# Performance work log

Measured on AMD Instinct MI355X. Metric: run time of the kernel, lower is better.

## Reference

```python
import jax, jax.numpy as jnp
import numpy as np

EPS = 1e-8  # torch F.cosine_similarity default eps


def setup_inputs() -> dict:
    key = jax.random.key(0)
    k1, k2 = jax.random.split(key)
    B, D, C = 8192, 1024, 1000
    x = jax.random.normal(k1, (B, D), dtype=jnp.float32)
    W = jax.random.normal(k2, (D, C), dtype=jnp.float32) * 0.02
    b = jnp.zeros((C,), dtype=jnp.float32)
    return {"x": x, "W": W, "b": b}


def reference(x, W, b):
    B = x.shape[0]
    # classifier logits -> softmax probs
    logits = x @ W + b                              # [B, C]
    logp = jax.nn.log_softmax(logits, axis=1)       # [B, C]
    pred = jnp.exp(logp)
    # per-row sum of p * log p (negative entropy), matches pred*log(pred) loop
    loss = jnp.sum(pred * logp, axis=-1)            # [B]
    # per-row mean cosine similarity against all rows (incl. self)
    norms = jnp.maximum(jnp.linalg.norm(x, axis=1, keepdims=True), EPS)
    xn = x / norms                                  # [B, D]
    sim = xn @ xn.T                                 # [B, B]
    weight = jnp.sum(sim, axis=1) / B               # [B]
    return loss * weight
```

## Files before the change

### kernel.cpp

```cpp
#include <hip/hip_runtime.h>
#include <hip/hip_bf16.h>
#include <cstdint>
#include <cstddef>

typedef __attribute__((ext_vector_type(8))) short bf16x8;
typedef __attribute__((ext_vector_type(4))) float f32x4;

__device__ __forceinline__ unsigned short f2bf(float f) {
  union { float f; unsigned u; } v; v.f = f;
  unsigned r = v.u + 0x7FFFu + ((v.u >> 16) & 1u);
  return (unsigned short)(r >> 16);
}

__device__ __forceinline__ float bf2f(unsigned short h) {
  union { float f; unsigned u; } c; c.u = ((unsigned)h) << 16;
  return c.f;
}

__device__ __forceinline__ void gload_lds16(const void* g, void* l) {
  __builtin_amdgcn_global_load_lds(
      (const __attribute__((address_space(1))) unsigned int*)g,
      (__attribute__((address_space(3))) unsigned int*)l, 16, 0, 0);
}

__global__ __launch_bounds__(1024) void k01_prep(const float* __restrict__ W,
                                                 unsigned short* __restrict__ Wt,
                                                 const float* __restrict__ x,
                                                 unsigned short* __restrict__ xbf,
                                                 float* __restrict__ rnorm,
                                                 float* __restrict__ sp) {
  __shared__ __align__(16) char sm[82176];
  int tid = threadIdx.x;
  int b = blockIdx.x;
  int lane = tid & 63;
  int wid = tid >> 6;

  int k0 = (b & 15) * 64;
  int c0 = (b >> 4) * 64;
  int tx = tid & 63;
  int ty = tid >> 6;
  float wreg[4];
#pragma unroll
  for (int i = 0; i < 4; ++i) {
    int c = c0 + tx;
    wreg[i] = (c < 1000) ? W[(size_t)(k0 + i * 16 + ty) * 1000 + c] : 0.f;
  }

  {
    float (*sblk)[1024] = (float(*)[1024])sm;
    int row0 = b * 32 + wid * 2;
    const float4* xr0 = (const float4*)(x + (size_t)row0 * 1024);
    const float4* xr1 = (const float4*)(x + (size_t)(row0 + 1) * 1024);
    float4 v[2][4];
#pragma unroll
    for (int j = 0; j < 4; ++j) v[0][j] = xr0[lane + j * 64];
#pragma unroll
    for (int j = 0; j < 4; ++j) v[1][j] = xr1[lane + j * 64];
    float ss0 = 0.f, ss1 = 0.f;
#pragma unroll
    for (int j = 0; j < 4; ++j) {
      ss0 += v[0][j].x * v[0][j].x + v[0][j].y * v[0][j].y +
             v[0][j].z * v[0][j].z + v[0][j].w * v[0][j].w;
      ss1 += v[1][j].x * v[1][j].x + v[1][j].y * v[1][j].y +
             v[1][j].z * v[1][j].z + v[1][j].w * v[1][j].w;
    }
#pragma unroll
    for (int m = 1; m < 64; m <<= 1) {
      ss0 += __shfl_xor(ss0, m);
      ss1 += __shfl_xor(ss1, m);
    }
    float rn0 = 1.f / fmaxf(sqrtf(ss0), 1e-8f);
    float rn1 = 1.f / fmaxf(sqrtf(ss1), 1e-8f);
    if (lane == 0) {
      rnorm[row0] = rn0;
      rnorm[row0 + 1] = rn1;
    }
    float4 sacc[4];
#pragma unroll
    for (int j = 0; j < 4; ++j) {
      ushort4 h0, h1;
      h0.x = f2bf(v[0][j].x); h0.y = f2bf(v[0][j].y);
      h0.z = f2bf(v[0][j].z); h0.w = f2bf(v[0][j].w);
      h1.x = f2bf(v[1][j].x); h1.y = f2bf(v[1][j].y);
      h1.z = f2bf(v[1][j].z); h1.w = f2bf(v[1][j].w);
      ((ushort4*)(xbf + (size_t)row0 * 1024))[lane + j * 64] = h0;
      ((ushort4*)(xbf + (size_t)(row0 + 1) * 1024))[lane + j * 64] = h1;
      sacc[j].x = v[0][j].x * rn0 + v[1][j].x * rn1;
      sacc[j].y = v[0][j].y * rn0 + v[1][j].y * rn1;
      sacc[j].z = v[0][j].z * rn0 + v[1][j].z * rn1;
      sacc[j].w = v[0][j].w * rn0 + v[1][j].w * rn1;
    }
#pragma unroll
    for (int j = 0; j < 4; ++j) ((float4*)sblk[wid])[j * 64 + lane] = sacc[j];
    __syncthreads();
    float acc = 0.f;
#pragma unroll
    for (int w = 0; w < 16; ++w) acc += sblk[w][tid];
    sp[(size_t)b * 1024 + tid] = acc;
  }

  {
    float (*tile)[65] = (float(*)[65])(sm + 65536);
#pragma unroll
    for (int i = 0; i < 4; ++i) tile[i * 16 + ty][tx] = wreg[i];
    __syncthreads();
#pragma unroll
    for (int i = 0; i < 4; ++i) {
      int ct = i * 16 + ty;
      Wt[(size_t)(c0 + ct) * 1024 + (k0 + tx)] = f2bf(tile[tx][ct]);
    }
  }
}

__global__ __launch_bounds__(256) void k2_sred(const float* __restrict__ sp,
                                               float* __restrict__ s) {
  __shared__ float red[4][64];
  int t = threadIdx.x;
  int dd = t & 63;
  int g = t >> 6;
  int d = blockIdx.x * 64 + dd;
  float acc = 0.f;
#pragma unroll 8
  for (int b = g * 64; b < g * 64 + 64; ++b) acc += sp[(size_t)b * 1024 + d];
  red[g][dd] = acc;
  __syncthreads();
  if (g == 0) s[d] = red[0][dd] + red[1][dd] + red[2][dd] + red[3][dd];
}

__global__ __launch_bounds__(256) void k3_gemm(const unsigned short* __restrict__ xbf,
                                               const unsigned short* __restrict__ wt,
                                               const float* __restrict__ bias,
                                               float* __restrict__ pm,
                                               float* __restrict__ pz,
                                               float* __restrict__ ps) {
  __shared__ __align__(16) char lds[65536];

  int tid = threadIdx.x;
  int lane = tid & 63;
  int wid = tid >> 6;
  int wc = wid & 1;
  int wr = wid >> 1;
  int cb = blockIdx.x >> 6;
  int rb = blockIdx.x & 63;
  int C0 = cb * 128;
  int R0 = rb * 128;

  float bv[4][4];
#pragma unroll
  for (int mf = 0; mf < 4; ++mf)
#pragma unroll
    for (int q = 0; q < 4; ++q) {
      int cls_g = C0 + wc * 64 + mf * 16 + (lane >> 4) * 4 + q;
      bv[mf][q] = (cls_g < 1000) ? bias[cls_g] : -1e30f;
    }
  f32x4 acc[4][4];
#pragma unroll
  for (int mf = 0; mf < 4; ++mf)
#pragma unroll
    for (int nf = 0; nf < 4; ++nf)
#pragma unroll
      for (int q = 0; q < 4; ++q) acc[mf][nf][q] = bv[mf][q];

  const char* gA = (const char*)(wt + (size_t)C0 * 1024);
  const char* gB = (const char*)(xbf + (size_t)R0 * 1024);
  int grow = (tid >> 3) & 7;
  int gswz = ((tid & 7) ^ grow) << 4;

  auto stage = [&](int kt, int bb) {
    char* lA = lds + bb * 32768;
    char* lB = lA + 16384;
#pragma unroll
    for (int i = 0; i < 4; ++i) {
      size_t row = i * 32 + (tid >> 3);
      gload_lds16(gA + row * 2048 + kt * 128 + gswz, lA + i * 4096 + tid * 16);
    }
#pragma unroll
    for (int i = 0; i < 4; ++i) {
      size_t row = i * 32 + (tid >> 3);
      gload_lds16(gB + row * 2048 + kt * 128 + gswz, lB + i * 4096 + tid * 16);
    }
  };

  int rsw = (lane & 7) << 4;
  int kcol = (lane >> 4) * 16;

  stage(0, 0);
  __syncthreads();
  int cur = 0;
  for (int t = 0; t < 16; ++t) {
    if (t < 15) stage(t + 1, cur ^ 1);
    const char* A = lds + cur * 32768;
    const char* B = A + 16384;
    bf16x8 a[4][2], bb[4][2];
#pragma unroll
    for (int mf = 0; mf < 4; ++mf)
#pragma unroll
      for (int ks = 0; ks < 2; ++ks)
        a[mf][ks] = *(const bf16x8*)(A + (wc * 64 + mf * 16 + (lane & 15)) * 128 +
                                     ((ks * 64 + kcol) ^ rsw));
#pragma unroll
    for (int nf = 0; nf < 4; ++nf)
#pragma unroll
      for (int ks = 0; ks < 2; ++ks)
        bb[nf][ks] = *(const bf16x8*)(B + (wr * 64 + nf * 16 + (lane & 15)) * 128 +
                                      ((ks * 64 + kcol) ^ rsw));
    __builtin_amdgcn_s_setprio(1);
#pragma unroll
    for (int ks = 0; ks < 2; ++ks)
#pragma unroll
      for (int mf = 0; mf < 4; ++mf)
#pragma unroll
        for (int nf = 0; nf < 4; ++nf)
          acc[mf][nf] = __builtin_amdgcn_mfma_f32_16x16x32_bf16(a[mf][ks], bb[nf][ks],
                                                                acc[mf][nf], 0, 0, 0);
    __builtin_amdgcn_s_setprio(0);
    __syncthreads();
    cur ^= 1;
  }

  float* mm = (float*)lds;
  float* zz = mm + 256;
  float* sv = zz + 256;
#pragma unroll
  for (int nf = 0; nf < 4; ++nf) {
    float m1 = -1e30f;
#pragma unroll
    for (int mf = 0; mf < 4; ++mf)
#pragma unroll
      for (int q = 0; q < 4; ++q) m1 = fmaxf(m1, acc[mf][nf][q]);
    m1 = fmaxf(m1, __shfl_xor(m1, 16));
    m1 = fmaxf(m1, __shfl_xor(m1, 32));
    float z1 = 0.f, s1 = 0.f;
#pragma unroll
    for (int mf = 0; mf < 4; ++mf)
#pragma unroll
      for (int q = 0; q < 4; ++q) {
        float tt = acc[mf][nf][q] - m1;
        float e = expf(tt);
        z1 += e;
        s1 += e * tt;
      }
    z1 += __shfl_xor(z1, 16); z1 += __shfl_xor(z1, 32);
    s1 += __shfl_xor(s1, 16); s1 += __shfl_xor(s1, 32);
    if (lane < 16) {
      int r = wr * 64 + nf * 16 + lane;
      mm[wc * 128 + r] = m1;
      zz[wc * 128 + r] = z1;
      sv[wc * 128 + r] = s1;
    }
  }
  __syncthreads();
  if (tid < 128) {
    float m0 = mm[tid], mA = mm[128 + tid];
    float z0 = zz[tid], zA = zz[128 + tid];
    float s0 = sv[tid], sA = sv[128 + tid];
    float M = fmaxf(m0, mA);
    float e0 = expf(m0 - M), e1 = expf(mA - M);
    float Z = z0 * e0 + zA * e1;
    float S = e0 * (s0 + (m0 - M) * z0) + e1 * (sA + (mA - M) * zA);
    size_t o = (size_t)cb * 8192 + R0 + tid;
    pm[o] = M;
    pz[o] = Z;
    ps[o] = S;
  }
}

__global__ __launch_bounds__(256) void k4_final(const unsigned short* __restrict__ xbf,
                                                const float* __restrict__ s,
                                                const float* __restrict__ rnorm,
                                                const float* __restrict__ pm,
                                                const float* __restrict__ pz,
                                                const float* __restrict__ ps,
                                                float* __restrict__ out) {
  int tid = threadIdx.x;
  int wid = tid >> 6, lane = tid & 63;
  int row = blockIdx.x * 4 + wid;
  const bf16x8* xr = (const bf16x8*)(xbf + (size_t)row * 1024);
  const float4* s4 = (const float4*)s;
  float dot = 0.f;
#pragma unroll
  for (int j = 0; j < 2; ++j) {
    bf16x8 v = xr[lane + j * 64];
    float4 sa = s4[(lane + j * 64) * 2];
    float4 sb = s4[(lane + j * 64) * 2 + 1];
    dot += bf2f((unsigned short)v[0]) * sa.x + bf2f((unsigned short)v[1]) * sa.y +
           bf2f((unsigned short)v[2]) * sa.z + bf2f((unsigned short)v[3]) * sa.w +
           bf2f((unsigned short)v[4]) * sb.x + bf2f((unsigned short)v[5]) * sb.y +
           bf2f((unsigned short)v[6]) * sb.z + bf2f((unsigned short)v[7]) * sb.w;
  }
#pragma unroll
  for (int m = 1; m < 64; m <<= 1) dot += __shfl_xor(dot, m);
  if (lane == 0) {
    float mv[8], zv[8], svv[8];
    float M = -1e30f;
#pragma unroll
    for (int c = 0; c < 8; ++c) {
      mv[c] = pm[(size_t)c * 8192 + row];
      zv[c] = pz[(size_t)c * 8192 + row];
      svv[c] = ps[(size_t)c * 8192 + row];
      M = fmaxf(M, mv[c]);
    }
    float Z = 0.f, S = 0.f;
#pragma unroll
    for (int c = 0; c < 8; ++c) {
      float e = expf(mv[c] - M);
      Z += zv[c] * e;
      S += e * (svv[c] + (mv[c] - M) * zv[c]);
    }
    float loss = S / Z - logf(Z);
    out[row] = loss * dot * rnorm[row] * (1.f / 8192.f);
  }
}

extern "C" void kernel_launch(void* const* d_in, const int* in_sizes, int n_in,
                              void* d_out, int out_size, void* d_ws, size_t ws_size,
                              hipStream_t stream) {
  (void)in_sizes; (void)n_in; (void)out_size; (void)ws_size;
  const float* x = (const float*)d_in[0];
  const float* W = (const float*)d_in[1];
  const float* b = (const float*)d_in[2];
  float* out = (float*)d_out;
  char* ws = (char*)d_ws;

  unsigned short* Wt = (unsigned short*)(ws + 0);
  unsigned short* xbf = (unsigned short*)(ws + 2097152);
  float* rnorm = (float*)(ws + 18874368);
  float* s = (float*)(ws + 18907136);
  float* sp = (float*)(ws + 18915328);
  float* pm = (float*)(ws + 18915328);
  float* pz = (float*)(ws + 18915328 + 262144);
  float* ps = (float*)(ws + 18915328 + 524288);

  k01_prep<<<256, 1024, 0, stream>>>(W, Wt, x, xbf, rnorm, sp);
  k2_sred<<<16, 256, 0, stream>>>(sp, s);
  k3_gemm<<<512, 256, 0, stream>>>(xbf, Wt, b, pm, pz, ps);
  k4_final<<<2048, 256, 0, stream>>>(xbf, s, rnorm, pm, pz, ps, out);
}
```

Measured before the change: 52.58 us.

## Pre-pack W into MFMA fragment layout and load A operand directly from global

The prep kernel now writes the transposed bf16 weights in a per-fragment layout, so each lane's 16-byte MFMA A operand is contiguous in global memory. The GEMM kernel drops LDS staging for the weight operand and loads A fragments straight from global/L2, which halves LDS use and removes the A global-to-LDS copies and LDS reads. The risk is that the direct global loads are not double-buffered, so their latency may be exposed in the main loop, and every wave in a block now fetches its own A fragments instead of sharing one staged copy.

```diff
diff --git a/kernel.cpp b/kernel.cpp
--- a/kernel.cpp
+++ b/kernel.cpp
@@ -24,12 +24,12 @@
 }
 
 __global__ __launch_bounds__(1024) void k01_prep(const float* __restrict__ W,
-                                                 unsigned short* __restrict__ Wt,
+                                                 unsigned short* __restrict__ wtf,
                                                  const float* __restrict__ x,
                                                  unsigned short* __restrict__ xbf,
                                                  float* __restrict__ rnorm,
                                                  float* __restrict__ sp) {
-  __shared__ __align__(16) char sm[82176];
+  __shared__ __align__(16) char sm[83968];
   int tid = threadIdx.x;
   int b = blockIdx.x;
   int lane = tid & 63;
@@ -100,14 +100,26 @@
   }
 
   {
-    float (*tile)[65] = (float(*)[65])(sm + 65536);
-#pragma unroll
-    for (int i = 0; i < 4; ++i) tile[i * 16 + ty][tx] = wreg[i];
+    float (*tile2)[72] = (float(*)[72])(sm + 65536);
+#pragma unroll
+    for (int i = 0; i < 4; ++i) tile2[tx][i * 16 + ty] = wreg[i];
     __syncthreads();
-#pragma unroll
-    for (int i = 0; i < 4; ++i) {
-      int ct = i * 16 + ty;
-      Wt[(size_t)(c0 + ct) * 1024 + (k0 + tx)] = f2bf(tile[tx][ct]);
+    if (tid < 512) {
+      int fi = tid >> 6;
+      int l = tid & 63;
+      int cf = fi >> 1;
+      int kf = fi & 1;
+      int r2 = cf * 16 + (l & 15);
+      int c2 = kf * 32 + (l >> 4) * 8;
+      float4 va = *(const float4*)&tile2[r2][c2];
+      float4 vb = *(const float4*)&tile2[r2][c2 + 4];
+      uint4 o;
+      o.x = (unsigned)f2bf(va.x) | ((unsigned)f2bf(va.y) << 16);
+      o.y = (unsigned)f2bf(va.z) | ((unsigned)f2bf(va.w) << 16);
+      o.z = (unsigned)f2bf(vb.x) | ((unsigned)f2bf(vb.y) << 16);
+      o.w = (unsigned)f2bf(vb.z) | ((unsigned)f2bf(vb.w) << 16);
+      size_t fg = (size_t)(c0 / 16 + cf) * 32 + (k0 / 32 + kf);
+      *(uint4*)((char*)wtf + fg * 1024 + (size_t)l * 16) = o;
     }
   }
 }
@@ -128,12 +140,12 @@
 }
 
 __global__ __launch_bounds__(256) void k3_gemm(const unsigned short* __restrict__ xbf,
-                                               const unsigned short* __restrict__ wt,
+                                               const unsigned short* __restrict__ wtf,
                                                const float* __restrict__ bias,
                                                float* __restrict__ pm,
                                                float* __restrict__ pz,
                                                float* __restrict__ ps) {
-  __shared__ __align__(16) char lds[65536];
+  __shared__ __align__(16) char lds[32768];
 
   int tid = threadIdx.x;
   int lane = tid & 63;
@@ -161,19 +173,12 @@
 #pragma unroll
       for (int q = 0; q < 4; ++q) acc[mf][nf][q] = bv[mf][q];
 
-  const char* gA = (const char*)(wt + (size_t)C0 * 1024);
   const char* gB = (const char*)(xbf + (size_t)R0 * 1024);
   int grow = (tid >> 3) & 7;
   int gswz = ((tid & 7) ^ grow) << 4;
 
-  auto stage = [&](int kt, int bb) {
-    char* lA = lds + bb * 32768;
-    char* lB = lA + 16384;
-#pragma unroll
-    for (int i = 0; i < 4; ++i) {
-      size_t row = i * 32 + (tid >> 3);
-      gload_lds16(gA + row * 2048 + kt * 128 + gswz, lA + i * 4096 + tid * 16);
-    }
+  auto stageB = [&](int kt, int bb) {
+    char* lB = lds + bb * 16384;
 #pragma unroll
     for (int i = 0; i < 4; ++i) {
       size_t row = i * 32 + (tid >> 3);
@@ -181,23 +186,24 @@
     }
   };
 
+  const char* gAf = (const char*)wtf +
+                    ((size_t)(cb * 8 + wc * 4) * 32) * 1024 + (size_t)lane * 16;
+
   int rsw = (lane & 7) << 4;
   int kcol = (lane >> 4) * 16;
 
-  stage(0, 0);
+  stageB(0, 0);
   __syncthreads();
   int cur = 0;
   for (int t = 0; t < 16; ++t) {
-    if (t < 15) stage(t + 1, cur ^ 1);
-    const char* A = lds + cur * 32768;
-    const char* B = A + 16384;
+    if (t < 15) stageB(t + 1, cur ^ 1);
     bf16x8 a[4][2], bb[4][2];
 #pragma unroll
     for (int mf = 0; mf < 4; ++mf)
 #pragma unroll
       for (int ks = 0; ks < 2; ++ks)
-        a[mf][ks] = *(const bf16x8*)(A + (wc * 64 + mf * 16 + (lane & 15)) * 128 +
-                                     ((ks * 64 + kcol) ^ rsw));
+        a[mf][ks] = *(const bf16x8*)(gAf + (size_t)(mf * 32 + t * 2 + ks) * 1024);
+    const char* B = lds + cur * 16384;
 #pragma unroll
     for (int nf = 0; nf < 4; ++nf)
 #pragma unroll
@@ -322,7 +328,7 @@
   float* out = (float*)d_out;
   char* ws = (char*)d_ws;
 
-  unsigned short* Wt = (unsigned short*)(ws + 0);
+  unsigned short* wtf = (unsigned short*)(ws + 0);
   unsigned short* xbf = (unsigned short*)(ws + 2097152);
   float* rnorm = (float*)(ws + 18874368);
   float* s = (float*)(ws + 18907136);
@@ -331,8 +337,8 @@
   float* pz = (float*)(ws + 18915328 + 262144);
   float* ps = (float*)(ws + 18915328 + 524288);
 
-  k01_prep<<<256, 1024, 0, stream>>>(W, Wt, x, xbf, rnorm, sp);
+  k01_prep<<<256, 1024, 0, stream>>>(W, wtf, x, xbf, rnorm, sp);
   k2_sred<<<16, 256, 0, stream>>>(sp, s);
-  k3_gemm<<<512, 256, 0, stream>>>(xbf, Wt, b, pm, pz, ps);
+  k3_gemm<<<512, 256, 0, stream>>>(xbf, wtf, b, pm, pz, ps);
   k4_final<<<2048, 256, 0, stream>>>(xbf, s, rnorm, pm, pz, ps, out);
 }
```

New measurement: 54.14 us. +3.0%, slower.

## Fold column-sum dot product into logits GEMM as extra class row

Applied to the files above, without the earlier changes.

The column sum vector s is written as bf16 into padding row 1000 of the transposed weight matrix, so the logits GEMM also computes x·s for every row in an otherwise unused class slot. That value is extracted before the softmax reductions and masked out. The final kernel then only combines the partial softmax stats with the precomputed dot, so it no longer re-reads the bf16 x matrix. This relies on Wt padding rows existing and on the bias-slot initialisation handling class 1000, and it adds one extra barrier in the GEMM epilogue.

```diff
diff --git a/kernel.cpp b/kernel.cpp
--- a/kernel.cpp
+++ b/kernel.cpp
@@ -113,7 +113,8 @@
 }
 
 __global__ __launch_bounds__(256) void k2_sred(const float* __restrict__ sp,
-                                               float* __restrict__ s) {
+                                               float* __restrict__ s,
+                                               unsigned short* __restrict__ Wt) {
   __shared__ float red[4][64];
   int t = threadIdx.x;
   int dd = t & 63;
@@ -124,7 +125,11 @@
   for (int b = g * 64; b < g * 64 + 64; ++b) acc += sp[(size_t)b * 1024 + d];
   red[g][dd] = acc;
   __syncthreads();
-  if (g == 0) s[d] = red[0][dd] + red[1][dd] + red[2][dd] + red[3][dd];
+  if (g == 0) {
+    float sv = red[0][dd] + red[1][dd] + red[2][dd] + red[3][dd];
+    s[d] = sv;
+    Wt[(size_t)1000 * 1024 + d] = f2bf(sv);
+  }
 }
 
 __global__ __launch_bounds__(256) void k3_gemm(const unsigned short* __restrict__ xbf,
@@ -132,7 +137,8 @@
                                                const float* __restrict__ bias,
                                                float* __restrict__ pm,
                                                float* __restrict__ pz,
-                                               float* __restrict__ ps) {
+                                               float* __restrict__ ps,
+                                               float* __restrict__ pd) {
   __shared__ __align__(16) char lds[65536];
 
   int tid = threadIdx.x;
@@ -151,7 +157,7 @@
 #pragma unroll
     for (int q = 0; q < 4; ++q) {
       int cls_g = C0 + wc * 64 + mf * 16 + (lane >> 4) * 4 + q;
-      bv[mf][q] = (cls_g < 1000) ? bias[cls_g] : -1e30f;
+      bv[mf][q] = (cls_g < 1000) ? bias[cls_g] : ((cls_g == 1000) ? 0.f : -1e30f);
     }
   f32x4 acc[4][4];
 #pragma unroll
@@ -218,9 +224,19 @@
     cur ^= 1;
   }
 
+  if (cb == 7 && wc == 1 && ((lane >> 4) == 2)) {
+#pragma unroll
+    for (int nf = 0; nf < 4; ++nf) {
+      int r = wr * 64 + nf * 16 + (lane & 15);
+      pd[(size_t)rb * 128 + r] = acc[2][nf][0];
+      acc[2][nf][0] = -1e30f;
+    }
+  }
+
   float* mm = (float*)lds;
   float* zz = mm + 256;
   float* sv = zz + 256;
+  __syncthreads();
 #pragma unroll
   for (int nf = 0; nf < 4; ++nf) {
     float m1 = -1e30f;
@@ -265,51 +281,31 @@
   }
 }
 
-__global__ __launch_bounds__(256) void k4_final(const unsigned short* __restrict__ xbf,
-                                                const float* __restrict__ s,
-                                                const float* __restrict__ rnorm,
+__global__ __launch_bounds__(256) void k4_final(const float* __restrict__ rnorm,
                                                 const float* __restrict__ pm,
                                                 const float* __restrict__ pz,
                                                 const float* __restrict__ ps,
+                                                const float* __restrict__ pd,
                                                 float* __restrict__ out) {
-  int tid = threadIdx.x;
-  int wid = tid >> 6, lane = tid & 63;
-  int row = blockIdx.x * 4 + wid;
-  const bf16x8* xr = (const bf16x8*)(xbf + (size_t)row * 1024);
-  const float4* s4 = (const float4*)s;
-  float dot = 0.f;
-#pragma unroll
-  for (int j = 0; j < 2; ++j) {
-    bf16x8 v = xr[lane + j * 64];
-    float4 sa = s4[(lane + j * 64) * 2];
-    float4 sb = s4[(lane + j * 64) * 2 + 1];
-    dot += bf2f((unsigned short)v[0]) * sa.x + bf2f((unsigned short)v[1]) * sa.y +
-           bf2f((unsigned short)v[2]) * sa.z + bf2f((unsigned short)v[3]) * sa.w +
-           bf2f((unsigned short)v[4]) * sb.x + bf2f((unsigned short)v[5]) * sb.y +
-           bf2f((unsigned short)v[6]) * sb.z + bf2f((unsigned short)v[7]) * sb.w;
-  }
-#pragma unroll
-  for (int m = 1; m < 64; m <<= 1) dot += __shfl_xor(dot, m);
-  if (lane == 0) {
-    float mv[8], zv[8], svv[8];
-    float M = -1e30f;
-#pragma unroll
-    for (int c = 0; c < 8; ++c) {
-      mv[c] = pm[(size_t)c * 8192 + row];
-      zv[c] = pz[(size_t)c * 8192 + row];
-      svv[c] = ps[(size_t)c * 8192 + row];
-      M = fmaxf(M, mv[c]);
-    }
-    float Z = 0.f, S = 0.f;
-#pragma unroll
-    for (int c = 0; c < 8; ++c) {
-      float e = expf(mv[c] - M);
-      Z += zv[c] * e;
-      S += e * (svv[c] + (mv[c] - M) * zv[c]);
-    }
-    float loss = S / Z - logf(Z);
-    out[row] = loss * dot * rnorm[row] * (1.f / 8192.f);
-  }
+  int row = blockIdx.x * 256 + threadIdx.x;
+  float mv[8], zv[8], svv[8];
+  float M = -1e30f;
+#pragma unroll
+  for (int c = 0; c < 8; ++c) {
+    mv[c] = pm[(size_t)c * 8192 + row];
+    zv[c] = pz[(size_t)c * 8192 + row];
+    svv[c] = ps[(size_t)c * 8192 + row];
+    M = fmaxf(M, mv[c]);
+  }
+  float Z = 0.f, S = 0.f;
+#pragma unroll
+  for (int c = 0; c < 8; ++c) {
+    float e = expf(mv[c] - M);
+    Z += zv[c] * e;
+    S += e * (svv[c] + (mv[c] - M) * zv[c]);
+  }
+  float loss = S / Z - logf(Z);
+  out[row] = loss * pd[row] * rnorm[row] * (1.f / 8192.f);
 }
 
 extern "C" void kernel_launch(void* const* d_in, const int* in_sizes, int n_in,
@@ -330,9 +326,10 @@
   float* pm = (float*)(ws + 18915328);
   float* pz = (float*)(ws + 18915328 + 262144);
   float* ps = (float*)(ws + 18915328 + 524288);
+  float* pd = (float*)(ws + 18915328 + 786432);
 
   k01_prep<<<256, 1024, 0, stream>>>(W, Wt, x, xbf, rnorm, sp);
-  k2_sred<<<16, 256, 0, stream>>>(sp, s);
-  k3_gemm<<<512, 256, 0, stream>>>(xbf, Wt, b, pm, pz, ps);
-  k4_final<<<2048, 256, 0, stream>>>(xbf, s, rnorm, pm, pz, ps, out);
-}
+  k2_sred<<<16, 256, 0, stream>>>(sp, s, Wt);
+  k3_gemm<<<512, 256, 0, stream>>>(xbf, Wt, b, pm, pz, ps, pd);
+  k4_final<<<32, 256, 0, stream>>>(rnorm, pm, pz, ps, pd, out);
+}
```

Result: faster. 48.95 us (-6.9%).
